# Kernel tuning notes

Measured on AMD Instinct MI355X. Metric: run time of the kernel, lower is better.

## Reference

```python
import jax, jax.numpy as jnp
import numpy as np

NUM_HEADS = 8
KEY_DIM = 16
D_V = 32  # attn_ratio * key_dim


def _conv1x1_bn(x, w, s, b):
    # x: [B, Cin, H, W], w: [Cout, Cin]; 1x1 conv == channel contraction,
    # eval-mode BatchNorm folded into per-channel scale s and bias b.
    y = jnp.einsum('bchw,oc->bohw', x, w)
    return y * s[:, None, None] + b[:, None, None]


def setup_inputs() -> dict:
    key = jax.random.key(0)
    ks = jax.random.split(key, 14)
    B, C, H, W = 16, 256, 32, 32
    nh_kd, dh = NUM_HEADS * KEY_DIM, NUM_HEADS * D_V
    f = jax.random.normal
    return {
        'x': f(ks[0], (B, C, H, W), jnp.float32),
        'wq': f(ks[1], (nh_kd, C), jnp.float32) * 0.05,
        'sq': jax.random.uniform(ks[2], (nh_kd,), jnp.float32),
        'bq': f(ks[3], (nh_kd,), jnp.float32) * 0.05,
        'wk': f(ks[4], (nh_kd, C), jnp.float32) * 0.05,
        'sk': jax.random.uniform(ks[5], (nh_kd,), jnp.float32),
        'bk': f(ks[6], (nh_kd,), jnp.float32) * 0.05,
        'wv': f(ks[7], (dh, C), jnp.float32) * 0.05,
        'sv': jax.random.uniform(ks[8], (dh,), jnp.float32),
        'bv': f(ks[9], (dh,), jnp.float32) * 0.05,
        'wp': f(ks[10], (C, dh), jnp.float32) * 0.05,
        'sp': jax.random.uniform(ks[11], (C,), jnp.float32),
        'bp': f(ks[12], (C,), jnp.float32) * 0.05,
    }


def reference(x, wq, sq, bq, wk, sk, bk, wv, sv, bv, wp, sp, bp):
    B, C, H, W = x.shape
    N = H * W
    # QKV projections (1x1 conv + folded BN)
    q = _conv1x1_bn(x, wq, sq, bq).reshape(B, NUM_HEADS, KEY_DIM, N)  # b h k n
    k = _conv1x1_bn(x, wk, sk, bk).reshape(B, NUM_HEADS, KEY_DIM, N)  # b h k m
    v = _conv1x1_bn(x, wv, sv, bv).reshape(B, NUM_HEADS, D_V, N)      # b h d m
    # NOTE: the original forward does NOT apply self.scale to the scores.
    attn = jnp.einsum('bhkn,bhkm->bhnm', q, k)
    attn = jax.nn.softmax(attn, axis=-1)
    out = jnp.einsum('bhnm,bhdm->bhdn', attn, v)  # b h d n
    out = out.reshape(B, NUM_HEADS * D_V, H, W)
    # proj = Sequential(activation, Conv2d_BN): activation FIRST
    out = jax.nn.relu(out)
    return _conv1x1_bn(out, wp, sp, bp)
```

## Files before the change

kernel.cpp:

```cpp
#include <hip/hip_runtime.h>

#define NTOT 1024
#define CIN  256
#define BATCH 16
#define NH   8
#define KD   16
#define DV   32
#define L2E  1.44269504088896340736f

typedef unsigned short u16;
typedef unsigned int   u32;
typedef __attribute__((ext_vector_type(2)))  _Float16 f16x2;
typedef __attribute__((ext_vector_type(8)))  _Float16 f16x8;
typedef __attribute__((ext_vector_type(16))) float    f32x16;

__device__ inline f16x8 as_f16x8(uint4 u) { return __builtin_bit_cast(f16x8, u); }
__device__ inline f16x2 as_f16x2(u32 u)   { return __builtin_bit_cast(f16x2, u); }
__device__ inline u32 pkrtz(float a, float b) {
  return __builtin_bit_cast(u32, __builtin_amdgcn_cvt_pkrtz(a, b));
}
__device__ inline u16 f2h(float x) {
  return __builtin_bit_cast(u16, (_Float16)x);
}
__device__ inline float fexp2(float x) {
#if __has_builtin(__builtin_amdgcn_exp2f)
  return __builtin_amdgcn_exp2f(x);
#else
  float r; asm("v_exp_f32 %0, %1" : "=v"(r) : "v"(x)); return r;
#endif
}
__device__ inline float dot2acc(u32 p2, float c) {
#if __has_builtin(__builtin_amdgcn_fdot2)
  const f16x2 one2 = __builtin_bit_cast(f16x2, (u32)0x3C003C00u);
  return __builtin_amdgcn_fdot2(as_f16x2(p2), one2, c, false);
#else
  const f16x2 v = as_f16x2(p2);
  return c + (float)v[0] + (float)v[1];
#endif
}

__global__ __launch_bounds__(256) void prep_fused(
    const float* __restrict__ X, u16* __restrict__ Xt,
    const float* __restrict__ wq, const float* __restrict__ sq, const float* __restrict__ bq,
    const float* __restrict__ wk, const float* __restrict__ sk, const float* __restrict__ bk,
    const float* __restrict__ wv, const float* __restrict__ sv, const float* __restrict__ bv,
    const float* __restrict__ wp, const float* __restrict__ sp, const float* __restrict__ bp,
    u16* __restrict__ wqkv, u16* __restrict__ wph, float* __restrict__ ball)
{
  __shared__ u16 T[64][64];
  const int bx = blockIdx.x;
  const int t  = threadIdx.x;
  if (bx < 1024) {
    const int n0 = (bx & 15) * 64;
    const int c0 = ((bx >> 4) & 3) * 64;
    const int b  = bx >> 6;
    #pragma unroll
    for (int rr = 0; rr < 4; ++rr) {
      const int c  = rr*16 + (t>>4);
      const int n4 = (t&15)*4;
      const float4 v = *(const float4*)&X[((size_t)b*CIN + c0 + c)*NTOT + n0 + n4];
      ushort4 r; r.x=f2h(v.x); r.y=f2h(v.y); r.z=f2h(v.z); r.w=f2h(v.w);
      *(ushort4*)&T[c][n4] = r;
    }
    __syncthreads();
    const int nl = t & 63;
    #pragma unroll
    for (int j = 0; j < 2; ++j) {
      const int oct = (t>>6)*2 + j;
      uint4 w;
      w.x = (u32)T[oct*8+0][nl] | ((u32)T[oct*8+1][nl] << 16);
      w.y = (u32)T[oct*8+2][nl] | ((u32)T[oct*8+3][nl] << 16);
      w.z = (u32)T[oct*8+4][nl] | ((u32)T[oct*8+5][nl] << 16);
      w.w = (u32)T[oct*8+6][nl] | ((u32)T[oct*8+7][nl] << 16);
      *(uint4*)&Xt[((size_t)b*NTOT + n0 + nl)*CIN + c0 + oct*8] = w;
    }
  } else {
    const int row = (bx - 1024)*4 + (t>>6);
    const int ln  = t & 63;
    const float* src; u16* dst; float sc, bi;
    if (row < 128)      { src = wq + (size_t)row*CIN;       sc = sq[row]*L2E;     bi = bq[row]*L2E;     dst = wqkv + (size_t)row*CIN; }
    else if (row < 256) { src = wk + (size_t)(row-128)*CIN; sc = sk[row-128];     bi = bk[row-128];     dst = wqkv + (size_t)row*CIN; }
    else if (row < 512) { src = wv + (size_t)(row-256)*CIN; sc = sv[row-256];     bi = bv[row-256];     dst = wqkv + (size_t)row*CIN; }
    else                { src = wp + (size_t)(row-512)*CIN; sc = sp[row-512];     bi = bp[row-512];     dst = wph + (size_t)(row-512)*CIN; }
    const float4 v = *(const float4*)&src[ln*4];
    ushort4 r;
    r.x = f2h(v.x*sc); r.y = f2h(v.y*sc); r.z = f2h(v.z*sc); r.w = f2h(v.w*sc);
    *(ushort4*)&dst[ln*4] = r;
    if (ln == 0) ball[row] = bi;
  }
}

template<int BN, int MODE>
__global__ __launch_bounds__(256) void conv_mfma(
    const u16* __restrict__ Wh, const u16* __restrict__ Bt,
    const float* __restrict__ ball,
    u16* __restrict__ q_t, u16* __restrict__ k_t, u16* __restrict__ v_h,
    float* __restrict__ outp)
{
  constexpr int FN = BN / 64;
  constexpr int NB = BN / 32;
  __shared__ u16 A_lds[2][128 * 64];
  __shared__ u16 B_lds[2][BN * 64];
  const int t    = threadIdx.x;
  const int lane = t & 63;
  const int w    = t >> 6;
  const int wm = w >> 1, wn = w & 1;
  const int g = lane >> 5, nl = lane & 31;
  const int n0 = blockIdx.x * BN;
  const int m0 = blockIdx.y * 128;
  const int b  = blockIdx.z;

  f32x16 acc[2][FN] = {};
  uint4 rA[4], rB[NB];

  #pragma unroll
  for (int r = 0; r < 4; ++r) {
    const int idx = t + r*256, row = idx >> 3, ch = idx & 7;
    rA[r] = *(const uint4*)&Wh[(size_t)(m0+row)*CIN + ch*8];
  }
  #pragma unroll
  for (int r = 0; r < NB; ++r) {
    const int idx = t + r*256, row = idx >> 3, ch = idx & 7;
    rB[r] = *(const uint4*)&Bt[((size_t)b*NTOT + n0 + row)*CIN + ch*8];
  }
  #pragma unroll
  for (int r = 0; r < 4; ++r) {
    const int idx = t + r*256, row = idx >> 3, ch = idx & 7;
    *(uint4*)&A_lds[0][row*64 + ((ch ^ (row&7))*8)] = rA[r];
  }
  #pragma unroll
  for (int r = 0; r < NB; ++r) {
    const int idx = t + r*256, row = idx >> 3, ch = idx & 7;
    *(uint4*)&B_lds[0][row*64 + ((ch ^ (row&7))*8)] = rB[r];
  }
  __syncthreads();

  for (int it = 0; it < 4; ++it) {
    const int cur = it & 1;
    if (it < 3) {
      const int c0 = (it+1)*64;
      #pragma unroll
      for (int r = 0; r < 4; ++r) {
        const int idx = t + r*256, row = idx >> 3, ch = idx & 7;
        rA[r] = *(const uint4*)&Wh[(size_t)(m0+row)*CIN + c0 + ch*8];
      }
      #pragma unroll
      for (int r = 0; r < NB; ++r) {
        const int idx = t + r*256, row = idx >> 3, ch = idx & 7;
        rB[r] = *(const uint4*)&Bt[((size_t)b*NTOT + n0 + row)*CIN + c0 + ch*8];
      }
    }
    #pragma unroll
    for (int ks = 0; ks < 4; ++ks) {
      const int ch = 2*ks + g;
      f16x8 a[2], bb[FN];
      #pragma unroll
      for (int fi = 0; fi < 2; ++fi) {
        const int row = wm*64 + fi*32 + nl;
        a[fi] = as_f16x8(*(const uint4*)&A_lds[cur][row*64 + ((ch ^ (row&7))*8)]);
      }
      #pragma unroll
      for (int fj = 0; fj < FN; ++fj) {
        const int row = wn*(BN/2) + fj*32 + nl;
        bb[fj] = as_f16x8(*(const uint4*)&B_lds[cur][row*64 + ((ch ^ (row&7))*8)]);
      }
      #pragma unroll
      for (int fi = 0; fi < 2; ++fi)
        #pragma unroll
        for (int fj = 0; fj < FN; ++fj)
          acc[fi][fj] = __builtin_amdgcn_mfma_f32_32x32x16_f16(a[fi], bb[fj], acc[fi][fj], 0, 0, 0);
    }
    if (it < 3) {
      #pragma unroll
      for (int r = 0; r < 4; ++r) {
        const int idx = t + r*256, row = idx >> 3, ch = idx & 7;
        *(uint4*)&A_lds[cur^1][row*64 + ((ch ^ (row&7))*8)] = rA[r];
      }
      #pragma unroll
      for (int r = 0; r < NB; ++r) {
        const int idx = t + r*256, row = idx >> 3, ch = idx & 7;
        *(uint4*)&B_lds[cur^1][row*64 + ((ch ^ (row&7))*8)] = rB[r];
      }
      __syncthreads();
    }
  }

  #pragma unroll
  for (int fi = 0; fi < 2; ++fi) {
    #pragma unroll
    for (int fj = 0; fj < FN; ++fj) {
      const int n = n0 + wn*(BN/2) + fj*32 + nl;
      #pragma unroll
      for (int q = 0; q < 4; ++q) {
        const int ob = m0 + wm*64 + fi*32 + 8*q + 4*g;
        const float v0 = acc[fi][fj][4*q+0] + ball[ob+0];
        const float v1 = acc[fi][fj][4*q+1] + ball[ob+1];
        const float v2 = acc[fi][fj][4*q+2] + ball[ob+2];
        const float v3 = acc[fi][fj][4*q+3] + ball[ob+3];
        if (MODE == 0) {
          if (ob < 128) {
            const int h = ob >> 4, k0 = ob & 15;
            ushort4 r; r.x = f2h(v0); r.y = f2h(v1); r.z = f2h(v2); r.w = f2h(v3);
            *(ushort4*)&q_t[(((size_t)b*NH + h)*NTOT + n)*KD + k0] = r;
          } else if (ob < 256) {
            const int oo = ob - 128;
            const int h = oo >> 4, k0 = oo & 15;
            const int plane = k0 >> 3, j0 = k0 & 7;
            ushort4 r; r.x = f2h(v0); r.y = f2h(v1); r.z = f2h(v2); r.w = f2h(v3);
            *(ushort4*)&k_t[((((size_t)b*NH + h)*2 + plane)*NTOT + n)*8 + j0] = r;
          } else {
            const int oo = ob - 256;
            const int h = oo >> 5, d0 = oo & 31;
            const int mb = n >> 4, loc = n & 15;
            const int g2 = (loc >> 2) & 1;
            const int j  = (loc & 3) + ((loc >> 3) << 2);
            u16* vp = v_h + (((((size_t)b*NH + h)*64 + mb)*2 + g2)*32 + d0)*8 + j;
            vp[0*8] = f2h(v0);
            vp[1*8] = f2h(v1);
            vp[2*8] = f2h(v2);
            vp[3*8] = f2h(v3);
          }
        } else {
          float* op = outp + ((size_t)b*CIN + ob)*NTOT + n;
          op[0*NTOT] = v0; op[1*NTOT] = v1; op[2*NTOT] = v2; op[3*NTOT] = v3;
        }
      }
    }
  }
}

__global__ __launch_bounds__(1024) void attn_mfma(
    const u16* __restrict__ Qt,
    const u16* __restrict__ Kt,
    const u16* __restrict__ Vt,
    u16* __restrict__ Ot)
{
  __shared__ u16 K_lds[2*NTOT*8];
  __shared__ u16 V_lds[4096*8];
  const int t    = threadIdx.x;
  const int lane = t & 63;
  const int wave = t >> 6;
  const int bh   = blockIdx.x >> 1;
  const int half = blockIdx.x & 1;
  const int g = lane >> 5, nl = lane & 31;
  const int n0 = half*512 + wave*32;

  const u16* Kh = Kt + (size_t)bh*(2*NTOT*8);
  const u16* Vh = Vt + (size_t)bh*(4096*8);
  const u16* Qh = Qt + (size_t)bh*(NTOT*KD);

  #pragma unroll
  for (int r = 0; r < 2; ++r) {
    const int uu = r*1024 + t;
    *(uint4*)&K_lds[uu*8] = *(const uint4*)&Kh[uu*8];
  }
  #pragma unroll
  for (int r = 0; r < 4; ++r) {
    const int uu = r*1024 + t;
    *(uint4*)&V_lds[uu*8] = *(const uint4*)&Vh[uu*8];
  }

  const f16x8 qf = as_f16x8(*(const uint4*)&Qh[(size_t)(n0+nl)*KD + g*8]);
  __syncthreads();

  const f32x16 fzero = {};
  f32x16 acc = {};
  float l = 0.f;
  const char* Kb = (const char*)K_lds + g*16384 + nl*16;
  const char* Vb = (const char*)V_lds + g*512   + nl*16;

  f16x8 kf  = as_f16x8(*(const uint4*)(Kb));
  uint4 va0 = *(const uint4*)(Vb);
  uint4 va1 = *(const uint4*)(Vb + 1024);
  f32x16 s_cur = __builtin_amdgcn_mfma_f32_32x32x16_f16(kf, qf, fzero, 0, 0, 0);

  #pragma unroll 2
  for (int st = 0; st < 31; ++st) {
    const f16x8 kfn = as_f16x8(*(const uint4*)(Kb + (st+1)*512));
    __builtin_amdgcn_s_setprio(1);
    const f32x16 s_next = __builtin_amdgcn_mfma_f32_32x32x16_f16(kfn, qf, fzero, 0, 0, 0);
    __builtin_amdgcn_s_setprio(0);
    const uint4 nva0 = *(const uint4*)(Vb + (st+1)*2048);
    const uint4 nva1 = *(const uint4*)(Vb + (st+1)*2048 + 1024);

    float p[16];
    #pragma unroll
    for (int r = 0; r < 16; ++r) p[r] = fexp2(s_cur[r]);
    uint4 b0, b1;
    b0.x = pkrtz(p[0],  p[1]);  b0.y = pkrtz(p[2],  p[3]);
    b0.z = pkrtz(p[4],  p[5]);  b0.w = pkrtz(p[6],  p[7]);
    b1.x = pkrtz(p[8],  p[9]);  b1.y = pkrtz(p[10], p[11]);
    b1.z = pkrtz(p[12], p[13]); b1.w = pkrtz(p[14], p[15]);
    l = dot2acc(b0.x, l); l = dot2acc(b0.y, l);
    l = dot2acc(b0.z, l); l = dot2acc(b0.w, l);
    l = dot2acc(b1.x, l); l = dot2acc(b1.y, l);
    l = dot2acc(b1.z, l); l = dot2acc(b1.w, l);

    __builtin_amdgcn_s_setprio(1);
    acc = __builtin_amdgcn_mfma_f32_32x32x16_f16(as_f16x8(va0), as_f16x8(b0), acc, 0, 0, 0);
    acc = __builtin_amdgcn_mfma_f32_32x32x16_f16(as_f16x8(va1), as_f16x8(b1), acc, 0, 0, 0);
    __builtin_amdgcn_s_setprio(0);
    s_cur = s_next; va0 = nva0; va1 = nva1;
  }
  {
    float p[16];
    #pragma unroll
    for (int r = 0; r < 16; ++r) p[r] = fexp2(s_cur[r]);
    uint4 b0, b1;
    b0.x = pkrtz(p[0],  p[1]);  b0.y = pkrtz(p[2],  p[3]);
    b0.z = pkrtz(p[4],  p[5]);  b0.w = pkrtz(p[6],  p[7]);
    b1.x = pkrtz(p[8],  p[9]);  b1.y = pkrtz(p[10], p[11]);
    b1.z = pkrtz(p[12], p[13]); b1.w = pkrtz(p[14], p[15]);
    l = dot2acc(b0.x, l); l = dot2acc(b0.y, l);
    l = dot2acc(b0.z, l); l = dot2acc(b0.w, l);
    l = dot2acc(b1.x, l); l = dot2acc(b1.y, l);
    l = dot2acc(b1.z, l); l = dot2acc(b1.w, l);
    acc = __builtin_amdgcn_mfma_f32_32x32x16_f16(as_f16x8(va0), as_f16x8(b0), acc, 0, 0, 0);
    acc = __builtin_amdgcn_mfma_f32_32x32x16_f16(as_f16x8(va1), as_f16x8(b1), acc, 0, 0, 0);
  }

  const float lt = l + __shfl_xor(l, 32);
  const float rl = 1.0f / lt;
  const int b = bh >> 3, h = bh & 7;
  u16* op = Ot + ((size_t)b*NTOT + n0 + nl)*CIN + h*DV;
  #pragma unroll
  for (int q = 0; q < 4; ++q) {
    const float v0 = fmaxf(acc[4*q+0]*rl, 0.f);
    const float v1 = fmaxf(acc[4*q+1]*rl, 0.f);
    const float v2 = fmaxf(acc[4*q+2]*rl, 0.f);
    const float v3 = fmaxf(acc[4*q+3]*rl, 0.f);
    uint2 pk; pk.x = pkrtz(v0, v1); pk.y = pkrtz(v2, v3);
    *(uint2*)&op[8*q + 4*g] = pk;
  }
}

extern "C" void kernel_launch(void* const* d_in, const int* in_sizes, int n_in,
                              void* d_out, int out_size, void* d_ws, size_t ws_size,
                              hipStream_t stream) {
  const float* x  = (const float*)d_in[0];
  const float* wq = (const float*)d_in[1];
  const float* sq = (const float*)d_in[2];
  const float* bq = (const float*)d_in[3];
  const float* wk = (const float*)d_in[4];
  const float* sk = (const float*)d_in[5];
  const float* bk = (const float*)d_in[6];
  const float* wv = (const float*)d_in[7];
  const float* sv = (const float*)d_in[8];
  const float* bv = (const float*)d_in[9];
  const float* wp = (const float*)d_in[10];
  const float* sp = (const float*)d_in[11];
  const float* bp = (const float*)d_in[12];
  float* out = (float*)d_out;

  char* ws = (char*)d_ws;
  u16*   x_t  = (u16*)(ws);
  u16*   q_t  = (u16*)(ws + (8u  << 20));
  u16*   k_t  = (u16*)(ws + (12u << 20));
  u16*   v_h  = (u16*)(ws + (16u << 20));
  u16*   wqkv = (u16*)(ws + (24u << 20));
  u16*   wph  = (u16*)(ws + (24u << 20) + (256u << 10));
  float* ball = (float*)(ws + (24u << 20) + (384u << 10));

  prep_fused<<<dim3(1216), dim3(256), 0, stream>>>(
      x, x_t, wq, sq, bq, wk, sk, bk, wv, sv, bv, wp, sp, bp, wqkv, wph, ball);
  conv_mfma<128, 0><<<dim3(8, 4, 16), dim3(256), 0, stream>>>(
      wqkv, x_t, ball, q_t, k_t, v_h, nullptr);
  attn_mfma<<<dim3(256), dim3(1024), 0, stream>>>(q_t, k_t, v_h, x_t );
  conv_mfma<64, 1><<<dim3(16, 2, 16), dim3(256), 0, stream>>>(
      wph, x_t , ball + 512, nullptr, nullptr, nullptr, out);
}
```

Measured before the change: 57.08 us.

## Halve V LDS buffer with two-phase reload, remap blocks, simplify attention loop

The attention kernel now keeps only half of V in shared memory and reloads the second half between two phases, separated by barriers. This cuts LDS per block from 96KB to 64KB, and a min-blocks hint is added to launch_bounds. Block IDs are remapped to spread heads across XCDs. The software-pipelined S/V prefetch is replaced by a plain fully unrolled loop with split row-sum accumulators. The risks are extra barriers, a global V load stalled in the middle of the loop, and less overlap between MFMA and exp.

```diff
diff --git a/kernel.cpp b/kernel.cpp
--- a/kernel.cpp
+++ b/kernel.cpp
@@ -229,19 +229,21 @@
   }
 }
 
-__global__ __launch_bounds__(1024) void attn_mfma(
+__global__ __launch_bounds__(1024, 8) void attn_mfma(
     const u16* __restrict__ Qt,
     const u16* __restrict__ Kt,
     const u16* __restrict__ Vt,
     u16* __restrict__ Ot)
 {
   __shared__ u16 K_lds[2*NTOT*8];
-  __shared__ u16 V_lds[4096*8];
+  __shared__ u16 V_lds[2048*8];
   const int t    = threadIdx.x;
   const int lane = t & 63;
   const int wave = t >> 6;
-  const int bh   = blockIdx.x >> 1;
-  const int half = blockIdx.x & 1;
+  const int bid  = blockIdx.x;
+  const int wgid = (bid & 7)*32 + (bid >> 3);
+  const int bh   = wgid >> 1;
+  const int half = wgid & 1;
   const int g = lane >> 5, nl = lane & 31;
   const int n0 = half*512 + wave*32;
 
@@ -249,77 +251,68 @@
   const u16* Vh = Vt + (size_t)bh*(4096*8);
   const u16* Qh = Qt + (size_t)bh*(NTOT*KD);
 
-  #pragma unroll
-  for (int r = 0; r < 2; ++r) {
-    const int uu = r*1024 + t;
-    *(uint4*)&K_lds[uu*8] = *(const uint4*)&Kh[uu*8];
-  }
-  #pragma unroll
-  for (int r = 0; r < 4; ++r) {
-    const int uu = r*1024 + t;
-    *(uint4*)&V_lds[uu*8] = *(const uint4*)&Vh[uu*8];
-  }
+  *(uint4*)&K_lds[t*8]          = *(const uint4*)&Kh[t*8];
+  *(uint4*)&K_lds[(t+1024)*8]   = *(const uint4*)&Kh[(t+1024)*8];
+  *(uint4*)&V_lds[t*8]          = *(const uint4*)&Vh[t*8];
+  *(uint4*)&V_lds[(t+1024)*8]   = *(const uint4*)&Vh[(t+1024)*8];
 
   const f16x8 qf = as_f16x8(*(const uint4*)&Qh[(size_t)(n0+nl)*KD + g*8]);
   __syncthreads();
 
   const f32x16 fzero = {};
   f32x16 acc = {};
-  float l = 0.f;
-  const char* Kb = (const char*)K_lds + g*16384 + nl*16;
-  const char* Vb = (const char*)V_lds + g*512   + nl*16;
-
-  f16x8 kf  = as_f16x8(*(const uint4*)(Kb));
-  uint4 va0 = *(const uint4*)(Vb);
-  uint4 va1 = *(const uint4*)(Vb + 1024);
-  f32x16 s_cur = __builtin_amdgcn_mfma_f32_32x32x16_f16(kf, qf, fzero, 0, 0, 0);
-
-  #pragma unroll 2
-  for (int st = 0; st < 31; ++st) {
-    const f16x8 kfn = as_f16x8(*(const uint4*)(Kb + (st+1)*512));
-    __builtin_amdgcn_s_setprio(1);
-    const f32x16 s_next = __builtin_amdgcn_mfma_f32_32x32x16_f16(kfn, qf, fzero, 0, 0, 0);
-    __builtin_amdgcn_s_setprio(0);
-    const uint4 nva0 = *(const uint4*)(Vb + (st+1)*2048);
-    const uint4 nva1 = *(const uint4*)(Vb + (st+1)*2048 + 1024);
-
-    float p[16];
-    #pragma unroll
-    for (int r = 0; r < 16; ++r) p[r] = fexp2(s_cur[r]);
-    uint4 b0, b1;
-    b0.x = pkrtz(p[0],  p[1]);  b0.y = pkrtz(p[2],  p[3]);
-    b0.z = pkrtz(p[4],  p[5]);  b0.w = pkrtz(p[6],  p[7]);
-    b1.x = pkrtz(p[8],  p[9]);  b1.y = pkrtz(p[10], p[11]);
-    b1.z = pkrtz(p[12], p[13]); b1.w = pkrtz(p[14], p[15]);
-    l = dot2acc(b0.x, l); l = dot2acc(b0.y, l);
-    l = dot2acc(b0.z, l); l = dot2acc(b0.w, l);
-    l = dot2acc(b1.x, l); l = dot2acc(b1.y, l);
-    l = dot2acc(b1.z, l); l = dot2acc(b1.w, l);
-
-    __builtin_amdgcn_s_setprio(1);
-    acc = __builtin_amdgcn_mfma_f32_32x32x16_f16(as_f16x8(va0), as_f16x8(b0), acc, 0, 0, 0);
-    acc = __builtin_amdgcn_mfma_f32_32x32x16_f16(as_f16x8(va1), as_f16x8(b1), acc, 0, 0, 0);
-    __builtin_amdgcn_s_setprio(0);
-    s_cur = s_next; va0 = nva0; va1 = nva1;
-  }
-  {
-    float p[16];
-    #pragma unroll
-    for (int r = 0; r < 16; ++r) p[r] = fexp2(s_cur[r]);
-    uint4 b0, b1;
-    b0.x = pkrtz(p[0],  p[1]);  b0.y = pkrtz(p[2],  p[3]);
-    b0.z = pkrtz(p[4],  p[5]);  b0.w = pkrtz(p[6],  p[7]);
-    b1.x = pkrtz(p[8],  p[9]);  b1.y = pkrtz(p[10], p[11]);
-    b1.z = pkrtz(p[12], p[13]); b1.w = pkrtz(p[14], p[15]);
-    l = dot2acc(b0.x, l); l = dot2acc(b0.y, l);
-    l = dot2acc(b0.z, l); l = dot2acc(b0.w, l);
-    l = dot2acc(b1.x, l); l = dot2acc(b1.y, l);
-    l = dot2acc(b1.z, l); l = dot2acc(b1.w, l);
-    acc = __builtin_amdgcn_mfma_f32_32x32x16_f16(as_f16x8(va0), as_f16x8(b0), acc, 0, 0, 0);
-    acc = __builtin_amdgcn_mfma_f32_32x32x16_f16(as_f16x8(va1), as_f16x8(b1), acc, 0, 0, 0);
-  }
-
-  const float lt = l + __shfl_xor(l, 32);
+  float l0 = 0.f, l1 = 0.f;
+  const char* Kbase = (const char*)K_lds + g*16384 + nl*16;
+  const char* Vbase = (const char*)V_lds + g*512   + nl*16;
+
+  #pragma unroll 1
+  for (int ph = 0; ph < 2; ++ph) {
+    const char* Kb = Kbase + ph*8192;
+    #pragma unroll
+    for (int sl = 0; sl < 16; ++sl) {
+      const f16x8 kf = as_f16x8(*(const uint4*)(Kb + sl*512));
+      const f32x16 s = __builtin_amdgcn_mfma_f32_32x32x16_f16(kf, qf, fzero, 0, 0, 0);
+
+      uint4 pb0;
+      {
+        float p[8];
+        #pragma unroll
+        for (int r = 0; r < 8; ++r) p[r] = fexp2(s[r]);
+        pb0.x = pkrtz(p[0], p[1]); pb0.y = pkrtz(p[2], p[3]);
+        pb0.z = pkrtz(p[4], p[5]); pb0.w = pkrtz(p[6], p[7]);
+        l0 = dot2acc(pb0.x, l0); l1 = dot2acc(pb0.y, l1);
+        l0 = dot2acc(pb0.z, l0); l1 = dot2acc(pb0.w, l1);
+      }
+      uint4 pb1;
+      {
+        float p[8];
+        #pragma unroll
+        for (int r = 0; r < 8; ++r) p[r] = fexp2(s[8+r]);
+        pb1.x = pkrtz(p[0], p[1]); pb1.y = pkrtz(p[2], p[3]);
+        pb1.z = pkrtz(p[4], p[5]); pb1.w = pkrtz(p[6], p[7]);
+        l0 = dot2acc(pb1.x, l0); l1 = dot2acc(pb1.y, l1);
+        l0 = dot2acc(pb1.z, l0); l1 = dot2acc(pb1.w, l1);
+      }
+
+      const uint4 va0 = *(const uint4*)(Vbase + sl*2048);
+      const uint4 va1 = *(const uint4*)(Vbase + sl*2048 + 1024);
+      __builtin_amdgcn_s_setprio(1);
+      acc = __builtin_amdgcn_mfma_f32_32x32x16_f16(as_f16x8(va0), as_f16x8(pb0), acc, 0, 0, 0);
+      acc = __builtin_amdgcn_mfma_f32_32x32x16_f16(as_f16x8(va1), as_f16x8(pb1), acc, 0, 0, 0);
+      __builtin_amdgcn_s_setprio(0);
+    }
+    if (ph == 0) {
+      __syncthreads();
+      const uint4 nv0 = *(const uint4*)&Vh[(2048 + t)*8];
+      const uint4 nv1 = *(const uint4*)&Vh[(3072 + t)*8];
+      *(uint4*)&V_lds[t*8]        = nv0;
+      *(uint4*)&V_lds[(t+1024)*8] = nv1;
+      __syncthreads();
+    }
+  }
+
+  const float lp = l0 + l1;
+  const float lt = lp + __shfl_xor(lp, 32);
   const float rl = 1.0f / lt;
   const int b = bh >> 3, h = bh & 7;
   u16* op = Ot + ((size_t)b*NTOT + n0 + nl)*CIN + h*DV;
```

After: 102.6 us. +79.8%, slower.
